# Kernel optimization log

Hardware: AMD Instinct MI355X
Metric: run time of the kernel (lower is better)

Reference implementation:

```python
import jax, jax.numpy as jnp
import numpy as np

B, D, L, N, M, K = 256, 512, 196, 1024, 512, 10000  # batch, context, num_ctx, hidden, embed, vocab


def setup_inputs() -> dict:
    key = jax.random.key(0)
    ks = jax.random.split(key, 20)
    r = lambda k, s: jax.random.normal(k, s, dtype=jnp.float32) * 0.02
    return {
        "a_i": jax.random.normal(ks[0], (B, D, L), dtype=jnp.float32),
        "inp": jax.random.normal(ks[1], (B, 1, K), dtype=jnp.float32),
        "hn_prev": jax.random.normal(ks[2], (B, 1, N), dtype=jnp.float32),
        "cn_prev": jax.random.normal(ks[3], (B, 1, N), dtype=jnp.float32),
        "f_att_w": r(ks[4], (N + D,)),  # Linear(n+D -> 1), stored as a vector
        "f_att_b": r(ks[5], (1,)),
        "gate_w": r(ks[6], (N,)),       # Linear(n -> 1)
        "gate_b": r(ks[7], (1,)),
        "E_w": r(ks[8], (M, K)),        # torch Linear weight [out, in]
        "E_b": r(ks[9], (M,)),
        "W_ih": r(ks[10], (4 * N, D + N + M)),  # LSTM input->hidden (i,f,g,o)
        "W_hh": r(ks[11], (4 * N, N)),
        "b_ih": r(ks[12], (4 * N,)),
        "b_hh": r(ks[13], (4 * N,)),
        "Lh_w": r(ks[14], (M, N)),
        "Lh_b": r(ks[15], (M,)),
        "Lz_w": r(ks[16], (M, D)),
        "Lz_b": r(ks[17], (M,)),
        "Lo_w": r(ks[18], (K, M)),
        "Lo_b": r(ks[19], (K,)),
    }


def reference(a_i, inp, hn_prev, cn_prev,
              f_att_w, f_att_b, gate_w, gate_b,
              E_w, E_b, W_ih, W_hh, b_ih, b_hh,
              Lh_w, Lh_b, Lz_w, Lz_b, Lo_w, Lo_b):
    h = hn_prev[:, 0]  # [B, N]
    c = cn_prev[:, 0]  # [B, N]
    # --- additive attention: the 196-iteration torch loop batched into one einsum ---
    # cat((a_i[:,:,i], h)) @ f_att_w splits into the a-part and h-part of the weight.
    w_a, w_h = f_att_w[:D], f_att_w[D:]
    e = jnp.einsum('bdl,d->bl', a_i, w_a) + (h @ w_h)[:, None] + f_att_b  # [B, L]
    alpha = jax.nn.softmax(e, axis=1)                                     # [B, L]
    beta = jax.nn.sigmoid(h @ gate_w + gate_b)                            # [B]
    z = beta[:, None] * jnp.einsum('bl,bdl->bd', alpha, a_i)              # [B, D]
    # --- word embedding ---
    w_emb = inp[:, 0] @ E_w.T + E_b                                       # [B, M]
    # --- single-step LSTM (PyTorch gate order i, f, g, o) ---
    x = jnp.concatenate([w_emb, h, z], axis=1)                            # [B, M+N+D]
    gates = x @ W_ih.T + b_ih + h @ W_hh.T + b_hh                         # [B, 4N]
    i_g, f_g, g_g, o_g = jnp.split(gates, 4, axis=1)
    cn = jax.nn.sigmoid(f_g) * c + jax.nn.sigmoid(i_g) * jnp.tanh(g_g)
    hn = jax.nn.sigmoid(o_g) * jnp.tanh(cn)
    # --- output projection ---
    deep_out = w_emb + (hn @ Lh_w.T + Lh_b) + (z @ Lz_w.T + Lz_b)         # [B, M]
    p_yt = deep_out @ Lo_w.T + Lo_b                                       # [B, K]
    return (p_yt[:, None, :], hn[:, None, :], cn[:, None, :], alpha[:, None, :])
```

## Files before the change

kernel.cpp:

```cpp
#include <hip/hip_runtime.h>
#include <hip/hip_bf16.h>
#include <math.h>

#define BB 256
#define DD 512
#define LL 196
#define NN 1024
#define MM 512
#define KK 10000

#define OUT_PY 0
#define OUT_HN ((size_t)2560000)
#define OUT_CN ((size_t)2822144)
#define OUT_AL ((size_t)3084288)

#define OFF_PE     ((size_t)0)
#define OFF_BETA   ((size_t)802816)
#define OFF_EMB    ((size_t)803072)
#define OFF_EMBP   ((size_t)934144)
#define OFF_GATESP ((size_t)3031296)
#define OFF_DP     ((size_t)11419904)
#define OFF_EWB    ((size_t)14565632)
#define OFF_WIHB   ((size_t)17125632)
#define OFF_WHHB   ((size_t)21319936)
#define OFF_LHB    ((size_t)23417088)
#define OFF_LZB    ((size_t)23679232)
#define OFF_LOB    ((size_t)23810304)
#define OFF_INPB   ((size_t)26370304)
#define OFF_HB     ((size_t)27650304)
#define OFF_ZB     ((size_t)27781376)
#define OFF_EMBB   ((size_t)27846912)
#define OFF_DEEPB  ((size_t)27912448)
#define OFF_HNB    ((size_t)27977984)

typedef __attribute__((ext_vector_type(8))) short short8v;
typedef __attribute__((ext_vector_type(4))) float f32x4;

__device__ __forceinline__ unsigned short f2bf(float f) {
    unsigned int u = __builtin_bit_cast(unsigned int, f);
    u += 0x7fffu + ((u >> 16) & 1u);
    return (unsigned short)(u >> 16);
}

__device__ __forceinline__ void gl_lds16(const float* g, float* l) {
    __builtin_amdgcn_global_load_lds(
        (const __attribute__((address_space(1))) void*)g,
        (__attribute__((address_space(3))) void*)l, 16, 0, 0);
}

__device__ __forceinline__ void cvt_body(int lb, const float* __restrict__ src,
                                         unsigned short* __restrict__ dst, int n,
                                         int t) {
#pragma unroll
    for (int i = 0; i < 8; ++i) {
        const size_t e = (size_t)lb * 16384 + (size_t)i * 2048 + (size_t)t * 8;
        if (e + 8 <= (size_t)n) {
            const float4 x = *(const float4*)(src + e);
            const float4 y = *(const float4*)(src + e + 4);
            short8v v;
            v[0] = (short)f2bf(x.x); v[1] = (short)f2bf(x.y);
            v[2] = (short)f2bf(x.z); v[3] = (short)f2bf(x.w);
            v[4] = (short)f2bf(y.x); v[5] = (short)f2bf(y.y);
            v[6] = (short)f2bf(y.z); v[7] = (short)f2bf(y.w);
            *(short8v*)(dst + e) = v;
        }
    }
}

__device__ __forceinline__ short8v stage8b(const unsigned short* __restrict__ p,
                                           bool ok, int kbase, int Ktot) {
    if (ok && (kbase + 7 < Ktot)) return *(const short8v*)(p + kbase);
    short8v v;
#pragma unroll
    for (int i = 0; i < 8; ++i) {
        const int k = kbase + i;
        v[i] = (ok && k < Ktot) ? (short)p[k] : (short)0;
    }
    return v;
}

struct GSrc { const unsigned short* A; int lda; const unsigned short* B; int ldb; int ktn; int K; };

__device__ __forceinline__ void gemm_body(
    const int bx, const int by, const int bz, const int rowBlocks,
    const GSrc s1, const GSrc s2,
    float* __restrict__ C, const int ldc, const int Ncols,
    const int ktPerSplit, const float* __restrict__ bias,
    short (*As)[64][72], short (*Bs)[64][72])
{
    const int t = threadIdx.x;
    const int row0 = bx * 64;
    const int col0 = by * 64;
    const int ktTot = s1.ktn + s2.ktn;
    const int kt0 = bz * ktPerSplit;
    const int nk = min(ktTot, kt0 + ktPerSplit) - kt0;

    const int sr = t >> 2;
    const int sk = (t & 3) << 4;
    const int bc = col0 + sr;
    const bool bok = (bc < Ncols);
    const unsigned short* aP1 = s1.A + (size_t)(row0 + sr) * s1.lda;
    const unsigned short* bP1 = s1.B + (size_t)(bok ? bc : 0) * s1.ldb;
    const unsigned short* aP2 = s2.A ? (s2.A + (size_t)(row0 + sr) * s2.lda) : aP1;
    const unsigned short* bP2 = s2.A ? (s2.B + (size_t)(bok ? bc : 0) * s2.ldb) : bP1;

    const int l = t & 63, w = t >> 6;
    const int wrow = (w >> 1) * 32, wcol = (w & 1) * 32;
    const int lr = l & 15, g = l >> 4, g8 = g * 8;

    f32x4 acc[2][2] = {};

    short8v sa0, sa1, sb0, sb1;
    {
        const int ktg = kt0;
        const unsigned short* aR; const unsigned short* bR; int kk, Kt;
        if (ktg < s1.ktn) { aR = aP1; bR = bP1; kk = (ktg << 6) + sk; Kt = s1.K; }
        else              { aR = aP2; bR = bP2; kk = ((ktg - s1.ktn) << 6) + sk; Kt = s2.K; }
        sa0 = stage8b(aR, true, kk, Kt);  sa1 = stage8b(aR, true, kk + 8, Kt);
        sb0 = stage8b(bR, bok,  kk, Kt);  sb1 = stage8b(bR, bok,  kk + 8, Kt);
    }
    *(short8v*)&As[0][sr][sk] = sa0; *(short8v*)&As[0][sr][sk + 8] = sa1;
    *(short8v*)&Bs[0][sr][sk] = sb0; *(short8v*)&Bs[0][sr][sk + 8] = sb1;
    __syncthreads();

    int cur = 0;
    for (int kt = 0; kt < nk; ++kt) {
        const bool more = (kt + 1 < nk);
        if (more) {
            const int ktg = kt0 + kt + 1;
            const unsigned short* aR; const unsigned short* bR; int kk, Kt;
            if (ktg < s1.ktn) { aR = aP1; bR = bP1; kk = (ktg << 6) + sk; Kt = s1.K; }
            else              { aR = aP2; bR = bP2; kk = ((ktg - s1.ktn) << 6) + sk; Kt = s2.K; }
            sa0 = stage8b(aR, true, kk, Kt);  sa1 = stage8b(aR, true, kk + 8, Kt);
            sb0 = stage8b(bR, bok,  kk, Kt);  sb1 = stage8b(bR, bok,  kk + 8, Kt);
        }
#pragma unroll
        for (int ks = 0; ks < 2; ++ks) {
            const int ko = ks * 32 + g8;
            short8v a0 = *(const short8v*)&As[cur][wrow + lr][ko];
            short8v a1 = *(const short8v*)&As[cur][wrow + 16 + lr][ko];
            short8v b0 = *(const short8v*)&Bs[cur][wcol + lr][ko];
            short8v b1 = *(const short8v*)&Bs[cur][wcol + 16 + lr][ko];
            acc[0][0] = __builtin_amdgcn_mfma_f32_16x16x32_bf16(a0, b0, acc[0][0], 0, 0, 0);
            acc[0][1] = __builtin_amdgcn_mfma_f32_16x16x32_bf16(a0, b1, acc[0][1], 0, 0, 0);
            acc[1][0] = __builtin_amdgcn_mfma_f32_16x16x32_bf16(a1, b0, acc[1][0], 0, 0, 0);
            acc[1][1] = __builtin_amdgcn_mfma_f32_16x16x32_bf16(a1, b1, acc[1][1], 0, 0, 0);
        }
        if (more) {
            *(short8v*)&As[cur ^ 1][sr][sk] = sa0;
            *(short8v*)&As[cur ^ 1][sr][sk + 8] = sa1;
            *(short8v*)&Bs[cur ^ 1][sr][sk] = sb0;
            *(short8v*)&Bs[cur ^ 1][sr][sk + 8] = sb1;
        }
        __syncthreads();
        cur ^= 1;
    }

    float* Cp = C + (size_t)bz * ((size_t)rowBlocks * 64) * ldc;
#pragma unroll
    for (int m = 0; m < 2; ++m)
#pragma unroll
        for (int n = 0; n < 2; ++n)
#pragma unroll
            for (int j = 0; j < 4; ++j) {
                const int r = row0 + wrow + m * 16 + g * 4 + j;
                const int c = col0 + wcol + n * 16 + lr;
                if (c < Ncols) {
                    float v = acc[m][n][j];
                    if (bias) v += bias[c];
                    Cp[(size_t)r * ldc + c] = v;
                }
            }
}

struct MegaP {
    const float *a_i, *inp, *h, *c_prev, *f_att_w, *f_att_b, *gate_w, *gate_b,
                *E_w, *E_b, *W_ih, *W_hh, *b_ih, *b_hh, *Lh_w, *Lh_b, *Lz_w,
                *Lz_b, *Lo_w, *Lo_b;
    float *alpha, *py, *hnout, *cnout;
    float *pe, *beta, *emb, *embp, *gatesp, *dp;
    unsigned short *ewb, *wihb, *whhb, *lhb, *lzb, *lob, *inpb, *hb, *zb,
                   *embb, *deepb, *hnb;
};


__device__ __forceinline__ void unit_p1(int u, int t, unsigned char* smem, const MegaP& p)
{
    if (u < 4096) {
        float* slab = (float*)smem;
        const int b = u >> 4, ch = u & 15;
        const int w = t >> 6, lane = t & 63;
        const float* gbase = p.a_i + ((size_t)b * DD + ch * 32) * LL;
#pragma unroll
        for (int k = 0; k < 7; ++k) {
            const int cw = k * 256 + w * 64;
            if (cw + lane < 1568)
                gl_lds16(gbase + (size_t)(cw + lane) * 4, slab + (size_t)cw * 4);
        }
        if (t < 8) slab[6272 + t] = 0.f;
        asm volatile("s_waitcnt vmcnt(0)" ::: "memory");
        __syncthreads();
        if (t < LL) {
            const float* wp = p.f_att_w + ch * 32;
            float e = 0.f;
#pragma unroll
            for (int d = 0; d < 32; ++d) e += slab[d * LL + t] * wp[d];
            p.pe[((size_t)b * 16 + ch) * LL + t] = e;
        }
    } else {
        int lb = u - 4096;
        if      (lb < 313) cvt_body(lb, p.E_w, p.ewb, 5120000, t);
        else if (lb < 470) cvt_body(lb - 313, p.inp, p.inpb, 2560000, t);
        else               cvt_body(lb - 470, p.h, p.hb, 262144, t);
    }
}

__device__ __forceinline__ void unit_p2(int u, int t, unsigned char* smem, const MegaP& p)
{
    if (u < 256) {
        const int b = u;
        float* red  = (float*)smem;
        float* red2 = red + 256;
        const float4 h4 = *(const float4*)(p.h + (size_t)b * NN + t * 4);
        const float4 w4 = *(const float4*)(p.f_att_w + DD + t * 4);
        const float4 g4 = *(const float4*)(p.gate_w + t * 4);
        float hd = h4.x * w4.x + h4.y * w4.y + h4.z * w4.z + h4.w * w4.w;
        float gd = h4.x * g4.x + h4.y * g4.y + h4.z * g4.z + h4.w * g4.w;
        red[t] = hd; red2[t] = gd;
        __syncthreads();
        for (int s = 128; s > 0; s >>= 1) {
            if (t < s) { red[t] += red[t + s]; red2[t] += red2[t + s]; }
            __syncthreads();
        }
        const float hdot = red[0];
        const float gdot = red2[0];
        __syncthreads();
        float e = -3.4e38f;
        if (t < LL) {
            const float* pp = p.pe + (size_t)b * 16 * LL + t;
            e = hdot + p.f_att_b[0];
#pragma unroll
            for (int ch = 0; ch < 16; ++ch) e += pp[ch * LL];
        }
        red[t] = e;
        __syncthreads();
        for (int s = 128; s > 0; s >>= 1) {
            if (t < s) red[t] = fmaxf(red[t], red[t + s]);
            __syncthreads();
        }
        const float mx = red[0];
        __syncthreads();
        const float ex = (t < LL) ? expf(e - mx) : 0.f;
        red[t] = ex;
        __syncthreads();
        for (int s = 128; s > 0; s >>= 1) {
            if (t < s) red[t] += red[t + s];
            __syncthreads();
        }
        const float inv = 1.f / red[0];
        if (t < LL) p.alpha[(size_t)b * LL + t] = ex * inv;
        if (t == 0) p.beta[b] = 1.f / (1.f + expf(-(gdot + p.gate_b[0])));
    } else if (u < 768) {
        short (*As)[64][72] = (short (*)[64][72])smem;
        short (*Bs)[64][72] = (short (*)[64][72])(smem + 18432);
        const int i = u - 256;
        GSrc s1 = {p.inpb, KK, p.ewb, KK, 157, KK};
        GSrc s2 = {nullptr, 0, nullptr, 0, 0, 0};
        gemm_body(i & 3, (i >> 2) & 7, i >> 5, 4, s1, s2,
                  p.embp, MM, MM, 10, nullptr, As, Bs);
    } else {
        int lb = u - 768;
        if (lb < 512) cvt_body(lb, p.W_ih, p.wihb, 8388608, t);
        else          cvt_body(lb - 512, p.W_hh, p.whhb, 4194304, t);
    }
}

__device__ __forceinline__ void unit_p3(int u, int t, unsigned char* smem, const MegaP& p)
{
    if (u < 4096) {
        float* slab = (float*)smem;
        float* al   = (float*)(smem + 25120);
        const int b = u >> 4, ch = u & 15;
        const int w = t >> 6, lane = t & 63;
        const float* gbase = p.a_i + ((size_t)b * DD + ch * 32) * LL;
#pragma unroll
        for (int k = 0; k < 7; ++k) {
            const int cw = k * 256 + w * 64;
            if (cw + lane < 1568)
                gl_lds16(gbase + (size_t)(cw + lane) * 4, slab + (size_t)cw * 4);
        }
        if (t < 200) al[t] = (t < LL) ? p.alpha[(size_t)b * LL + t] : 0.f;
        if (t < 8) slab[6272 + t] = 0.f;
        asm volatile("s_waitcnt vmcnt(0)" ::: "memory");
        __syncthreads();
        const int r = t >> 3, q = t & 7;
        const float* rowp = slab + r * LL + q * 25;
        const float* alq  = al + q * 25;
        float s = 0.f;
#pragma unroll
        for (int j = 0; j < 25; ++j) s += rowp[j] * alq[j];
        s += __shfl_xor(s, 1, 64);
        s += __shfl_xor(s, 2, 64);
        s += __shfl_xor(s, 4, 64);
        if (q == 0) p.zb[(size_t)b * DD + ch * 32 + r] = f2bf(p.beta[b] * s);
    } else if (u < 4608) {
        const int idx = (u - 4096) * 256 + t;
        const int j = idx & 511;
        float v = p.E_b[j];
#pragma unroll
        for (int s = 0; s < 16; ++s) v += p.embp[(size_t)s * (BB * 512) + idx];
        p.emb[idx] = v;
        p.embb[idx] = f2bf(v);
    } else {
        int lb = u - 4608;
        if      (lb < 313) cvt_body(lb, p.Lo_w, p.lob, 5120000, t);
        else if (lb < 345) cvt_body(lb - 313, p.Lh_w, p.lhb, 524288, t);
        else               cvt_body(lb - 345, p.Lz_w, p.lzb, 262144, t);
    }
}

__device__ __forceinline__ void unit_p4(int u, int t, unsigned char* smem, const MegaP& p)
{
    short (*As)[64][72] = (short (*)[64][72])smem;
    short (*Bs)[64][72] = (short (*)[64][72])(smem + 18432);
    if (u < 512) {
        GSrc s1 = {p.hb, NN, p.wihb + 512, 2048, 16, NN};
        GSrc s2 = {p.hb, NN, p.whhb, NN, 16, NN};
        gemm_body(u & 3, (u >> 2) & 63, u >> 8, 4, s1, s2,
                  p.gatesp, 4096, 4096, 16, nullptr, As, Bs);
    } else if (u < 1024) {
        const int i = u - 512;
        GSrc s1 = {p.embb, MM, p.wihb, 2048, 8, MM};
        GSrc s2 = {nullptr, 0, nullptr, 0, 0, 0};
        gemm_body(i & 3, (i >> 2) & 63, i >> 8, 4, s1, s2,
                  p.gatesp + (size_t)2 * BB * 4096, 4096, 4096, 4, nullptr, As, Bs);
    } else if (u < 1536) {
        const int i = u - 1024;
        GSrc s1 = {p.zb, DD, p.wihb + 1536, 2048, 8, DD};
        GSrc s2 = {nullptr, 0, nullptr, 0, 0, 0};
        gemm_body(i & 3, (i >> 2) & 63, i >> 8, 4, s1, s2,
                  p.gatesp + (size_t)4 * BB * 4096, 4096, 4096, 4, nullptr, As, Bs);
    } else {
        const int i = u - 1536;
        GSrc s1 = {p.zb, DD, p.lzb, DD, 8, DD};
        GSrc s2 = {nullptr, 0, nullptr, 0, 0, 0};
        gemm_body(i & 3, (i >> 2) & 7, i >> 5, 4, s1, s2,
                  p.dp, MM, MM, 1, nullptr, As, Bs);
    }
}

__device__ __forceinline__ void unit_p5(int u, int t, const MegaP& p)
{
    const int idx = u * 256 + t;
    const int b = idx >> 10, n = idx & 1023;
    float g[4];
#pragma unroll
    for (int gi = 0; gi < 4; ++gi) {
        const int col = gi * 1024 + n;
        const size_t o = (size_t)b * 4096 + col;
        float v = p.b_ih[col] + p.b_hh[col];
#pragma unroll
        for (int s = 0; s < 6; ++s) v += p.gatesp[(size_t)s * (BB * 4096) + o];
        g[gi] = v;
    }
    const float si = 1.f / (1.f + expf(-g[0]));
    const float sf = 1.f / (1.f + expf(-g[1]));
    const float so = 1.f / (1.f + expf(-g[3]));
    const float tg = tanhf(g[2]);
    const float c = p.c_prev[idx];
    const float cnv = sf * c + si * tg;
    const float hnv = so * tanhf(cnv);
    p.cnout[idx] = cnv;
    p.hnout[idx] = hnv;
    p.hnb[idx] = f2bf(hnv);
}

__device__ __forceinline__ void unit_p6(int u, int t, unsigned char* smem, const MegaP& p)
{
    short (*As)[64][72] = (short (*)[64][72])smem;
    short (*Bs)[64][72] = (short (*)[64][72])(smem + 18432);
    GSrc s1 = {p.hnb, NN, p.lhb, NN, 16, NN};
    GSrc s2 = {nullptr, 0, nullptr, 0, 0, 0};
    gemm_body(u & 3, (u >> 2) & 7, u >> 5, 4, s1, s2,
              p.dp + (size_t)8 * BB * 512, MM, MM, 1, nullptr, As, Bs);
}

__device__ __forceinline__ void unit_p7(int u, int t, const MegaP& p)
{
    const int idx = u * 256 + t;
    const int j = idx & 511;
    float v = p.emb[idx] + p.Lh_b[j] + p.Lz_b[j];
#pragma unroll
    for (int s = 0; s < 24; ++s) v += p.dp[(size_t)s * (BB * 512) + idx];
    p.deepb[idx] = f2bf(v);
}

__device__ __forceinline__ void unit_p8(int u, int t, unsigned char* smem, const MegaP& p)
{
    short (*As)[64][72] = (short (*)[64][72])smem;
    short (*Bs)[64][72] = (short (*)[64][72])(smem + 18432);
    GSrc s1 = {p.deepb, MM, p.lob, MM, 8, MM};
    GSrc s2 = {nullptr, 0, nullptr, 0, 0, 0};
    gemm_body(u & 3, u >> 2, 0, 4, s1, s2,
              p.py, KK, KK, 8, p.Lo_b, As, Bs);
}

__global__ __launch_bounds__(256) void gk_p1(MegaP p) {
    __shared__ __align__(16) unsigned char smem[36864];
    unit_p1(blockIdx.x, threadIdx.x, smem, p);
}
__global__ __launch_bounds__(256) void gk_p2(MegaP p) {
    __shared__ __align__(16) unsigned char smem[36864];
    unit_p2(blockIdx.x, threadIdx.x, smem, p);
}
__global__ __launch_bounds__(256) void gk_p3(MegaP p) {
    __shared__ __align__(16) unsigned char smem[36864];
    unit_p3(blockIdx.x, threadIdx.x, smem, p);
}
__global__ __launch_bounds__(256) void gk_p4(MegaP p) {
    __shared__ __align__(16) unsigned char smem[36864];
    unit_p4(blockIdx.x, threadIdx.x, smem, p);
}
__global__ __launch_bounds__(256) void gk_p5(MegaP p) {
    unit_p5(blockIdx.x, threadIdx.x, p);
}
__global__ __launch_bounds__(256) void gk_p6(MegaP p) {
    __shared__ __align__(16) unsigned char smem[36864];
    unit_p6(blockIdx.x, threadIdx.x, smem, p);
}
__global__ __launch_bounds__(256) void gk_p7(MegaP p) {
    unit_p7(blockIdx.x, threadIdx.x, p);
}
__global__ __launch_bounds__(256) void gk_p8(MegaP p) {
    __shared__ __align__(16) unsigned char smem[36864];
    unit_p8(blockIdx.x, threadIdx.x, smem, p);
}

extern "C" void kernel_launch(void* const* d_in, const int* in_sizes, int n_in,
                              void* d_out, int out_size, void* d_ws, size_t ws_size,
                              hipStream_t stream)
{
    float* out = (float*)d_out;
    float* ws  = (float*)d_ws;

    MegaP p;
    p.a_i     = (const float*)d_in[0];
    p.inp     = (const float*)d_in[1];
    p.h       = (const float*)d_in[2];
    p.c_prev  = (const float*)d_in[3];
    p.f_att_w = (const float*)d_in[4];
    p.f_att_b = (const float*)d_in[5];
    p.gate_w  = (const float*)d_in[6];
    p.gate_b  = (const float*)d_in[7];
    p.E_w     = (const float*)d_in[8];
    p.E_b     = (const float*)d_in[9];
    p.W_ih    = (const float*)d_in[10];
    p.W_hh    = (const float*)d_in[11];
    p.b_ih    = (const float*)d_in[12];
    p.b_hh    = (const float*)d_in[13];
    p.Lh_w    = (const float*)d_in[14];
    p.Lh_b    = (const float*)d_in[15];
    p.Lz_w    = (const float*)d_in[16];
    p.Lz_b    = (const float*)d_in[17];
    p.Lo_w    = (const float*)d_in[18];
    p.Lo_b    = (const float*)d_in[19];
    p.alpha   = out + OUT_AL;
    p.py      = out + OUT_PY;
    p.hnout   = out + OUT_HN;
    p.cnout   = out + OUT_CN;
    p.pe      = ws + OFF_PE;
    p.beta    = ws + OFF_BETA;
    p.emb     = ws + OFF_EMB;
    p.embp    = ws + OFF_EMBP;
    p.gatesp  = ws + OFF_GATESP;
    p.dp      = ws + OFF_DP;
    p.ewb     = (unsigned short*)(ws + OFF_EWB);
    p.wihb    = (unsigned short*)(ws + OFF_WIHB);
    p.whhb    = (unsigned short*)(ws + OFF_WHHB);
    p.lhb     = (unsigned short*)(ws + OFF_LHB);
    p.lzb     = (unsigned short*)(ws + OFF_LZB);
    p.lob     = (unsigned short*)(ws + OFF_LOB);
    p.inpb    = (unsigned short*)(ws + OFF_INPB);
    p.hb      = (unsigned short*)(ws + OFF_HB);
    p.zb      = (unsigned short*)(ws + OFF_ZB);
    p.embb    = (unsigned short*)(ws + OFF_EMBB);
    p.deepb   = (unsigned short*)(ws + OFF_DEEPB);
    p.hnb     = (unsigned short*)(ws + OFF_HNB);

    gk_p1<<<4582, 256, 0, stream>>>(p);
    gk_p2<<<1536, 256, 0, stream>>>(p);
    gk_p3<<<4969, 256, 0, stream>>>(p);
    gk_p4<<<1792, 256, 0, stream>>>(p);
    gk_p5<<<1024, 256, 0, stream>>>(p);
    gk_p6<<<512, 256, 0, stream>>>(p);
    gk_p7<<<512, 256, 0, stream>>>(p);
    gk_p8<<<628, 256, 0, stream>>>(p);
}
```

Measured before the change: 138.2 us.

## Replace split-K partial buffers with atomicAdd into zeroed accumulators

Split-K GEMM stages for the embedding, LSTM gates and deep-output projections now atomically add into a single accumulator buffer instead of writing one partial slab per split. The buffer is zeroed by extra blocks in the first kernel, and the reduction loops in later stages become single loads. This removes the write and re-read traffic of up to 24 partial slices, at the cost of atomic contention and non-deterministic summation order. Shared memory sizes for two kernels are also reduced, which may allow more blocks per CU.

```diff
diff --git a/kernel.cpp b/kernel.cpp
--- a/kernel.cpp
+++ b/kernel.cpp
@@ -17,9 +17,11 @@
 #define OFF_PE     ((size_t)0)
 #define OFF_BETA   ((size_t)802816)
 #define OFF_EMB    ((size_t)803072)
-#define OFF_EMBP   ((size_t)934144)
-#define OFF_GATESP ((size_t)3031296)
-#define OFF_DP     ((size_t)11419904)
+#define OFF_ACC    ((size_t)934144)
+#define OFF_EMBP1  (OFF_ACC)
+#define OFF_GATESP1 (OFF_ACC + 131072)
+#define OFF_DP1    (OFF_ACC + 1179648)
+#define ACC_FLOATS 1310720
 #define OFF_EWB    ((size_t)14565632)
 #define OFF_WIHB   ((size_t)17125632)
 #define OFF_WHHB   ((size_t)21319936)
@@ -85,7 +87,7 @@
     const int bx, const int by, const int bz, const int rowBlocks,
     const GSrc s1, const GSrc s2,
     float* __restrict__ C, const int ldc, const int Ncols,
-    const int ktPerSplit, const float* __restrict__ bias,
+    const int ktPerSplit, const float* __restrict__ bias, const int atomicOut,
     short (*As)[64][72], short (*Bs)[64][72])
 {
     const int t = threadIdx.x;
@@ -156,7 +158,8 @@
         cur ^= 1;
     }
 
-    float* Cp = C + (size_t)bz * ((size_t)rowBlocks * 64) * ldc;
+    float* Cp = C + (atomicOut ? (size_t)0
+                               : (size_t)bz * ((size_t)rowBlocks * 64) * ldc);
 #pragma unroll
     for (int m = 0; m < 2; ++m)
 #pragma unroll
@@ -168,7 +171,8 @@
                 if (c < Ncols) {
                     float v = acc[m][n][j];
                     if (bias) v += bias[c];
-                    Cp[(size_t)r * ldc + c] = v;
+                    if (atomicOut) atomicAdd(&Cp[(size_t)r * ldc + c], v);
+                    else           Cp[(size_t)r * ldc + c] = v;
                 }
             }
 }
@@ -178,7 +182,7 @@
                 *E_w, *E_b, *W_ih, *W_hh, *b_ih, *b_hh, *Lh_w, *Lh_b, *Lz_w,
                 *Lz_b, *Lo_w, *Lo_b;
     float *alpha, *py, *hnout, *cnout;
-    float *pe, *beta, *emb, *embp, *gatesp, *dp;
+    float *pe, *beta, *emb, *embp1, *gatesp1, *dp1, *accbase;
     unsigned short *ewb, *wihb, *whhb, *lhb, *lzb, *lob, *inpb, *hb, *zb,
                    *embb, *deepb, *hnb;
 };
@@ -207,11 +211,17 @@
             for (int d = 0; d < 32; ++d) e += slab[d * LL + t] * wp[d];
             p.pe[((size_t)b * 16 + ch) * LL + t] = e;
         }
-    } else {
+    } else if (u < 4582) {
         int lb = u - 4096;
         if      (lb < 313) cvt_body(lb, p.E_w, p.ewb, 5120000, t);
         else if (lb < 470) cvt_body(lb - 313, p.inp, p.inpb, 2560000, t);
         else               cvt_body(lb - 470, p.h, p.hb, 262144, t);
+    } else {
+        const int lb = u - 4582;
+        float* dst = p.accbase + (size_t)lb * 4096 + (size_t)t * 16;
+        const float4 zz = make_float4(0.f, 0.f, 0.f, 0.f);
+#pragma unroll
+        for (int i = 0; i < 4; ++i) *(float4*)(dst + i * 4) = zz;
     }
 }
 
@@ -267,7 +277,7 @@
         GSrc s1 = {p.inpb, KK, p.ewb, KK, 157, KK};
         GSrc s2 = {nullptr, 0, nullptr, 0, 0, 0};
         gemm_body(i & 3, (i >> 2) & 7, i >> 5, 4, s1, s2,
-                  p.embp, MM, MM, 10, nullptr, As, Bs);
+                  p.embp1, MM, MM, 10, nullptr, 1, As, Bs);
     } else {
         int lb = u - 768;
         if (lb < 512) cvt_body(lb, p.W_ih, p.wihb, 8388608, t);
@@ -306,9 +316,7 @@
     } else if (u < 4608) {
         const int idx = (u - 4096) * 256 + t;
         const int j = idx & 511;
-        float v = p.E_b[j];
-#pragma unroll
-        for (int s = 0; s < 16; ++s) v += p.embp[(size_t)s * (BB * 512) + idx];
+        const float v = p.E_b[j] + p.embp1[idx];
         p.emb[idx] = v;
         p.embb[idx] = f2bf(v);
     } else {
@@ -327,25 +335,25 @@
         GSrc s1 = {p.hb, NN, p.wihb + 512, 2048, 16, NN};
         GSrc s2 = {p.hb, NN, p.whhb, NN, 16, NN};
         gemm_body(u & 3, (u >> 2) & 63, u >> 8, 4, s1, s2,
-                  p.gatesp, 4096, 4096, 16, nullptr, As, Bs);
+                  p.gatesp1, 4096, 4096, 16, nullptr, 1, As, Bs);
     } else if (u < 1024) {
         const int i = u - 512;
         GSrc s1 = {p.embb, MM, p.wihb, 2048, 8, MM};
         GSrc s2 = {nullptr, 0, nullptr, 0, 0, 0};
         gemm_body(i & 3, (i >> 2) & 63, i >> 8, 4, s1, s2,
-                  p.gatesp + (size_t)2 * BB * 4096, 4096, 4096, 4, nullptr, As, Bs);
+                  p.gatesp1, 4096, 4096, 4, nullptr, 1, As, Bs);
     } else if (u < 1536) {
         const int i = u - 1024;
         GSrc s1 = {p.zb, DD, p.wihb + 1536, 2048, 8, DD};
         GSrc s2 = {nullptr, 0, nullptr, 0, 0, 0};
         gemm_body(i & 3, (i >> 2) & 63, i >> 8, 4, s1, s2,
-                  p.gatesp + (size_t)4 * BB * 4096, 4096, 4096, 4, nullptr, As, Bs);
+                  p.gatesp1, 4096, 4096, 4, nullptr, 1, As, Bs);
     } else {
         const int i = u - 1536;
         GSrc s1 = {p.zb, DD, p.lzb, DD, 8, DD};
         GSrc s2 = {nullptr, 0, nullptr, 0, 0, 0};
         gemm_body(i & 3, (i >> 2) & 7, i >> 5, 4, s1, s2,
-                  p.dp, MM, MM, 1, nullptr, As, Bs);
+                  p.dp1, MM, MM, 1, nullptr, 1, As, Bs);
     }
 }
 
@@ -357,11 +365,7 @@
 #pragma unroll
     for (int gi = 0; gi < 4; ++gi) {
         const int col = gi * 1024 + n;
-        const size_t o = (size_t)b * 4096 + col;
-        float v = p.b_ih[col] + p.b_hh[col];
-#pragma unroll
-        for (int s = 0; s < 6; ++s) v += p.gatesp[(size_t)s * (BB * 4096) + o];
-        g[gi] = v;
+        g[gi] = p.b_ih[col] + p.b_hh[col] + p.gatesp1[(size_t)b * 4096 + col];
     }
     const float si = 1.f / (1.f + expf(-g[0]));
     const float sf = 1.f / (1.f + expf(-g[1]));
@@ -382,16 +386,14 @@
     GSrc s1 = {p.hnb, NN, p.lhb, NN, 16, NN};
     GSrc s2 = {nullptr, 0, nullptr, 0, 0, 0};
     gemm_body(u & 3, (u >> 2) & 7, u >> 5, 4, s1, s2,
-              p.dp + (size_t)8 * BB * 512, MM, MM, 1, nullptr, As, Bs);
+              p.dp1, MM, MM, 1, nullptr, 1, As, Bs);
 }
 
 __device__ __forceinline__ void unit_p7(int u, int t, const MegaP& p)
 {
     const int idx = u * 256 + t;
     const int j = idx & 511;
-    float v = p.emb[idx] + p.Lh_b[j] + p.Lz_b[j];
-#pragma unroll
-    for (int s = 0; s < 24; ++s) v += p.dp[(size_t)s * (BB * 512) + idx];
+    const float v = p.emb[idx] + p.Lh_b[j] + p.Lz_b[j] + p.dp1[idx];
     p.deepb[idx] = f2bf(v);
 }
 
@@ -402,11 +404,11 @@
     GSrc s1 = {p.deepb, MM, p.lob, MM, 8, MM};
     GSrc s2 = {nullptr, 0, nullptr, 0, 0, 0};
     gemm_body(u & 3, u >> 2, 0, 4, s1, s2,
-              p.py, KK, KK, 8, p.Lo_b, As, Bs);
+              p.py, KK, KK, 8, p.Lo_b, 0, As, Bs);
 }
 
 __global__ __launch_bounds__(256) void gk_p1(MegaP p) {
-    __shared__ __align__(16) unsigned char smem[36864];
+    __shared__ __align__(16) unsigned char smem[25120];
     unit_p1(blockIdx.x, threadIdx.x, smem, p);
 }
 __global__ __launch_bounds__(256) void gk_p2(MegaP p) {
@@ -414,7 +416,7 @@
     unit_p2(blockIdx.x, threadIdx.x, smem, p);
 }
 __global__ __launch_bounds__(256) void gk_p3(MegaP p) {
-    __shared__ __align__(16) unsigned char smem[36864];
+    __shared__ __align__(16) unsigned char smem[25920];
     unit_p3(blockIdx.x, threadIdx.x, smem, p);
 }
 __global__ __launch_bounds__(256) void gk_p4(MegaP p) {
@@ -471,9 +473,10 @@
     p.pe      = ws + OFF_PE;
     p.beta    = ws + OFF_BETA;
     p.emb     = ws + OFF_EMB;
-    p.embp    = ws + OFF_EMBP;
-    p.gatesp  = ws + OFF_GATESP;
-    p.dp      = ws + OFF_DP;
+    p.embp1   = ws + OFF_EMBP1;
+    p.gatesp1 = ws + OFF_GATESP1;
+    p.dp1     = ws + OFF_DP1;
+    p.accbase = ws + OFF_ACC;
     p.ewb     = (unsigned short*)(ws + OFF_EWB);
     p.wihb    = (unsigned short*)(ws + OFF_WIHB);
     p.whhb    = (unsigned short*)(ws + OFF_WHHB);
@@ -487,7 +490,7 @@
     p.deepb   = (unsigned short*)(ws + OFF_DEEPB);
     p.hnb     = (unsigned short*)(ws + OFF_HNB);
 
-    gk_p1<<<4582, 256, 0, stream>>>(p);
+    gk_p1<<<4902, 256, 0, stream>>>(p);
     gk_p2<<<1536, 256, 0, stream>>>(p);
     gk_p3<<<4969, 256, 0, stream>>>(p);
     gk_p4<<<1792, 256, 0, stream>>>(p);
```

Measured after the change: 146.5 us. +6.0%, slower.
